# Kernel tuning notes

Measured on AMD Instinct MI355X. Metric: run time of the kernel, lower is better.

Reference implementation:

```python
import jax, jax.numpy as jnp
import numpy as np

H = 768
L = 9
M = 5            # max_span_length
CTX_RATIO = 0.5
NEG_INF = -1e30


def setup_inputs() -> dict:
    key = jax.random.key(0)
    ks = jax.random.split(key, 12)
    B, S = 4, 2048
    sc = 1.0 / np.sqrt(H)
    return {
        "sequence_output": jax.random.normal(ks[0], (B, S, H), dtype=jnp.float32),
        "Wc": jax.random.normal(ks[1], (H, L), dtype=jnp.float32) * sc,
        "bc": jnp.zeros((L,), dtype=jnp.float32),
        "wa": jax.random.normal(ks[2], (H,), dtype=jnp.float32) * sc,
        "ba": jnp.zeros((), dtype=jnp.float32),
        "W1": jax.random.normal(ks[3], (2 * H, H), dtype=jnp.float32) * (1.0 / np.sqrt(2 * H)),
        "b1": jnp.zeros((H,), dtype=jnp.float32),
        "gamma": jnp.ones((H,), dtype=jnp.float32),
        "beta": jnp.zeros((H,), dtype=jnp.float32),
        "W2": jax.random.normal(ks[4], (H, L), dtype=jnp.float32) * sc,
        "b2": jnp.zeros((L,), dtype=jnp.float32),
    }


def reference(sequence_output, Wc, bc, wa, ba, W1, b1, gamma, beta, W2, b2):
    x = sequence_output                        # [B,S,H]
    B, S, _ = x.shape
    base_logits = jnp.einsum('bsh,hl->bsl', x, Wc) + bc   # [B,S,L]

    # sliding-window indices: window [i-M, i+M] clipped to [0, S)
    offsets = jnp.arange(-M, M + 1)            # [W]
    idx = jnp.arange(S)[:, None] + offsets     # [S,W]
    valid = (idx >= 0) & (idx < S)             # [S,W]
    idx_c = jnp.clip(idx, 0, S - 1)            # [S,W]

    # attention scores over window (span_attention linear -> scalar per token)
    scores = jnp.einsum('bsh,h->bs', x, wa) + ba           # [B,S]
    win_scores = scores[:, idx_c]                          # [B,S,W]
    win_scores = jnp.where(valid[None], win_scores, NEG_INF)
    attn = jax.nn.softmax(win_scores, axis=-1)             # [B,S,W]

    win_tokens = x[:, idx_c]                               # [B,S,W,H] gather
    weighted_ctx = jnp.einsum('bsw,bswh->bsh', attn, win_tokens)

    token_with_ctx = jnp.concatenate([x, weighted_ctx], axis=-1)  # [B,S,2H]
    h = jnp.einsum('bsd,dh->bsh', token_with_ctx, W1) + b1
    # LayerNorm (eps = 1e-5, torch default)
    mu = jnp.mean(h, axis=-1, keepdims=True)
    var = jnp.mean((h - mu) ** 2, axis=-1, keepdims=True)
    h = (h - mu) * jax.lax.rsqrt(var + 1e-5) * gamma + beta
    h = jax.nn.gelu(h, approximate=False)                  # torch nn.GELU default (erf)
    ctx_logits = jnp.einsum('bsh,hl->bsl', h, W2) + b2

    return (1.0 - CTX_RATIO) * base_logits + CTX_RATIO * ctx_logits
```

## Files before the change

kernel.cpp:

```cpp
#include <hip/hip_runtime.h>
#include <hip/hip_bf16.h>
#include <math.h>

#define S_LEN 2048
#define BATCH 4
#define HDIM 768
#define LOUT 9
#define NROWS (BATCH*S_LEN)
#define K2H 1536
#define KHALF 768
#define WIN 11
#define NEG_INF_F (-1e30f)

typedef __attribute__((ext_vector_type(4))) float f32x4;
typedef __attribute__((ext_vector_type(8))) short bf16x8;

static __device__ __forceinline__ void async_ld16(const void* g, void* l) {
  __builtin_amdgcn_global_load_lds((const __attribute__((address_space(1))) void*)g,
                                   (__attribute__((address_space(3))) void*)l, 16, 0, 0);
}

static __device__ __forceinline__ unsigned short f2bf(float f) {
  union { float f; unsigned int u; } v; v.f = f;
  unsigned int u = v.u;
  unsigned int r = (u + 0x7fffu + ((u >> 16) & 1u)) >> 16;
  return (unsigned short)r;
}

static __device__ __forceinline__ float bf2f(unsigned short h) {
  union { unsigned int u; float f; } v; v.u = ((unsigned int)h) << 16;
  return v.f;
}

__global__ __launch_bounds__(256) void k_prep_w1t(const float* __restrict__ W1,
                                                  unsigned short* __restrict__ W1t) {
  __shared__ float tile[32][33];
  int bk = blockIdx.x % 48;
  int bn = blockIdx.x / 48;
  int tc = threadIdx.x % 32;
  int tr = threadIdx.x / 32;
  #pragma unroll
  for (int i = 0; i < 32; i += 8) {
    tile[tr + i][tc] = W1[(bk*32 + tr + i) * HDIM + bn*32 + tc];
  }
  __syncthreads();
  #pragma unroll
  for (int i = 0; i < 32; i += 8) {
    W1t[(bn*32 + tr + i) * K2H + bk*32 + tc] = f2bf(tile[tc][tr + i]);
  }
}

__global__ __launch_bounds__(192) void k_prep(const float* __restrict__ x,
                                              const float* __restrict__ wa,
                                              const float* __restrict__ ba,
                                              const float* __restrict__ Wc,
                                              const float* __restrict__ bc,
                                              unsigned short* __restrict__ xc,
                                              float* __restrict__ scores,
                                              float* __restrict__ base) {
  __shared__ float red[3][LOUT + 1];
  int bid = blockIdx.x;
  int row = (bid & 7) * 1024 + (bid >> 3);
  int t = threadIdx.x;
  int lane = t & 63, wave = t >> 6;
  const float4 v = *(const float4*)(x + row * HDIM + t * 4);
  const float4 w = *(const float4*)(wa + t * 4);
  ushort4 o;
  o.x = f2bf(v.x); o.y = f2bf(v.y); o.z = f2bf(v.z); o.w = f2bf(v.w);
  *(ushort4*)(xc + row * K2H + t * 4) = o;

  float pv[LOUT + 1];
  pv[LOUT] = v.x * w.x + v.y * w.y + v.z * w.z + v.w * w.w;
  #pragma unroll
  for (int l = 0; l < LOUT; ++l) pv[l] = 0.f;
  const float xvv[4] = { v.x, v.y, v.z, v.w };
  #pragma unroll
  for (int j = 0; j < 4; ++j) {
    const float* wr = Wc + (t * 4 + j) * LOUT;
    #pragma unroll
    for (int l = 0; l < LOUT; ++l) pv[l] += xvv[j] * wr[l];
  }
  #pragma unroll
  for (int l = 0; l <= LOUT; ++l)
    #pragma unroll
    for (int m = 1; m < 64; m <<= 1) pv[l] += __shfl_xor(pv[l], m);
  if (lane == 0) {
    #pragma unroll
    for (int l = 0; l <= LOUT; ++l) red[wave][l] = pv[l];
  }
  __syncthreads();
  if (t < LOUT) {
    base[row * LOUT + t] = red[0][t] + red[1][t] + red[2][t] + bc[t];
  } else if (t == LOUT) {
    scores[row] = red[0][LOUT] + red[1][LOUT] + red[2][LOUT] + ba[0];
  }
}

__global__ __launch_bounds__(192) void k_ctx(const float* __restrict__ scores,
                                             unsigned short* __restrict__ xc) {
  __shared__ float swin[WIN];
  int bid = blockIdx.x;
  int row = (bid & 7) * 1024 + (bid >> 3);
  int b = row >> 11, s = row & 2047;
  int t = threadIdx.x;
  if (t < WIN) {
    int j = s - 5 + t;
    bool valid = (j >= 0) && (j < S_LEN);
    int jc = valid ? j : (j < 0 ? 0 : S_LEN - 1);
    swin[t] = valid ? scores[b * S_LEN + jc] : NEG_INF_F;
  }
  __syncthreads();
  float mx = swin[0];
  #pragma unroll
  for (int w = 1; w < WIN; ++w) mx = fmaxf(mx, swin[w]);
  float es[WIN], ssum = 0.f;
  #pragma unroll
  for (int w = 0; w < WIN; ++w) {
    float sv = swin[w];
    es[w] = (sv > -1e29f) ? __expf(sv - mx) : 0.f;
    ssum += es[w];
  }
  float inv = 1.f / ssum;
  float c0 = 0.f, c1 = 0.f, c2 = 0.f, c3 = 0.f;
  #pragma unroll
  for (int w = 0; w < WIN; ++w) {
    float aw = es[w] * inv;
    int j = s - 5 + w;
    int jc = (j < 0) ? 0 : ((j >= S_LEN) ? S_LEN - 1 : j);
    const ushort4 uv = *(const ushort4*)(xc + (((long)b * S_LEN + jc) * K2H) + t * 4);
    c0 += aw * bf2f(uv.x);
    c1 += aw * bf2f(uv.y);
    c2 += aw * bf2f(uv.z);
    c3 += aw * bf2f(uv.w);
  }
  ushort4 o;
  o.x = f2bf(c0); o.y = f2bf(c1); o.z = f2bf(c2); o.w = f2bf(c3);
  *(ushort4*)(xc + row * K2H + HDIM + t * 4) = o;
}

__global__ __launch_bounds__(256, 3) void k_gemm(const unsigned short* __restrict__ A,
                                                 const unsigned short* __restrict__ Bt,
                                                 unsigned short* __restrict__ Hout) {
  __shared__ unsigned short As[2][128 * 32];
  __shared__ unsigned short Bs[2][128 * 32];
  int bid = blockIdx.x;
  int obid = (bid & 7) * 96 + (bid >> 3);
  int kh = obid / 384;
  int mt = obid % 384;
  int bm = mt / 6, bn = mt % 6;
  int t = threadIdx.x;
  int lane = t & 63, wave = t >> 6;
  int wm = wave >> 1, wn = wave & 1;

  int rowc = lane >> 2;
  int fST = ((lane >> 2) ^ (lane >> 4)) & 3;
  int sST = (lane & 3) ^ fST;
  const unsigned short* gA0 = A  + (long)(bm * 128 + wave * 16 + rowc) * K2H + kh * KHALF + sST * 8;
  const unsigned short* gB0 = Bt + (long)(bn * 128 + wave * 16 + rowc) * K2H + kh * KHALF + sST * 8;

  int fR = ((lane & 3) ^ ((lane >> 2) & 3)) & 3;
  int slR = ((lane >> 4) ^ fR) & 3;
  int arow = wm * 64 + (lane & 15);
  int brow = wn * 64 + (lane & 15);

  f32x4 acc[4][4] = {};

#define STAGE(buf, kt) do {                                                    \
    async_ld16(gA0 + (kt),            &As[buf][(wave * 16) * 32]);             \
    async_ld16(gA0 + 64 * K2H + (kt), &As[buf][(64 + wave * 16) * 32]);        \
    async_ld16(gB0 + (kt),            &Bs[buf][(wave * 16) * 32]);             \
    async_ld16(gB0 + 64 * K2H + (kt), &Bs[buf][(64 + wave * 16) * 32]);        \
  } while (0)

#define COMPUTE(buf) do {                                                      \
    bf16x8 af[4], bfv[4];                                                      \
    _Pragma("unroll")                                                          \
    for (int m = 0; m < 4; ++m)                                                \
      af[m] = *(const bf16x8*)(&As[buf][(arow + m * 16) * 32 + slR * 8]);      \
    _Pragma("unroll")                                                          \
    for (int n = 0; n < 4; ++n)                                                \
      bfv[n] = *(const bf16x8*)(&Bs[buf][(brow + n * 16) * 32 + slR * 8]);     \
    _Pragma("unroll")                                                          \
    for (int m = 0; m < 4; ++m)                                                \
      _Pragma("unroll")                                                        \
      for (int n = 0; n < 4; ++n)                                              \
        acc[m][n] = __builtin_amdgcn_mfma_f32_16x16x32_bf16(af[m], bfv[n], acc[m][n], 0, 0, 0); \
  } while (0)

  STAGE(0, 0);
  __syncthreads();
  int cur = 0;
  #pragma unroll 1
  for (int tt = 0; tt < 23; ++tt) {
    STAGE(cur ^ 1, (tt + 1) * 32);
    COMPUTE(cur);
    __syncthreads();
    cur ^= 1;
  }
  COMPUTE(cur);

  unsigned short* Hp = Hout + (long)kh * NROWS * HDIM;
  int orow = bm * 128 + wm * 64 + (lane >> 4) * 4;
  int ocol = bn * 128 + wn * 64 + (lane & 15);
  #pragma unroll
  for (int m = 0; m < 4; ++m)
    #pragma unroll
    for (int n = 0; n < 4; ++n) {
      int col = ocol + n * 16;
      #pragma unroll
      for (int r = 0; r < 4; ++r) {
        Hp[(long)(orow + m * 16 + r) * HDIM + col] = f2bf(acc[m][n][r]);
      }
    }
#undef STAGE
#undef COMPUTE
}

__global__ __launch_bounds__(192) void k_ln(const unsigned short* __restrict__ H0,
                                            const unsigned short* __restrict__ H1,
                                            const float* __restrict__ b1,
                                            const float* __restrict__ gamma,
                                            const float* __restrict__ beta,
                                            const float* __restrict__ W2,
                                            const float* __restrict__ b2,
                                            const float* __restrict__ base,
                                            float* __restrict__ out) {
  __shared__ float redS[3], redQ[3], redp[3][LOUT];
  int row = blockIdx.x;
  int t = threadIdx.x;
  int lane = t & 63, wave = t >> 6;
  const ushort4 h0 = *(const ushort4*)(H0 + (long)row * HDIM + t * 4);
  const ushort4 h1 = *(const ushort4*)(H1 + (long)row * HDIM + t * 4);
  const float4 b14 = *(const float4*)(b1 + t * 4);
  const float vv[4] = { bf2f(h0.x) + bf2f(h1.x) + b14.x,
                        bf2f(h0.y) + bf2f(h1.y) + b14.y,
                        bf2f(h0.z) + bf2f(h1.z) + b14.z,
                        bf2f(h0.w) + bf2f(h1.w) + b14.w };
  float s1 = vv[0] + vv[1] + vv[2] + vv[3];
  float s2 = vv[0]*vv[0] + vv[1]*vv[1] + vv[2]*vv[2] + vv[3]*vv[3];
  #pragma unroll
  for (int m = 1; m < 64; m <<= 1) { s1 += __shfl_xor(s1, m); s2 += __shfl_xor(s2, m); }
  if (lane == 0) { redS[wave] = s1; redQ[wave] = s2; }
  __syncthreads();
  s1 = redS[0] + redS[1] + redS[2];
  s2 = redQ[0] + redQ[1] + redQ[2];
  float mu = s1 * (1.f / HDIM);
  float var = s2 * (1.f / HDIM) - mu * mu;
  float rstd = rsqrtf(var + 1e-5f);
  const float4 g4 = *(const float4*)(gamma + t * 4);
  const float4 be4 = *(const float4*)(beta + t * 4);
  const float gv[4] = { g4.x, g4.y, g4.z, g4.w };
  const float bvv[4] = { be4.x, be4.y, be4.z, be4.w };
  float p[LOUT] = {};
  #pragma unroll
  for (int j = 0; j < 4; ++j) {
    float g = (vv[j] - mu) * rstd * gv[j] + bvv[j];
    float gg = 0.5f * g * (1.f + erff(g * 0.70710678118654752f));
    const float* wrow = W2 + (t * 4 + j) * LOUT;
    #pragma unroll
    for (int l = 0; l < LOUT; ++l) p[l] += gg * wrow[l];
  }
  #pragma unroll
  for (int l = 0; l < LOUT; ++l)
    #pragma unroll
    for (int m = 1; m < 64; m <<= 1) p[l] += __shfl_xor(p[l], m);
  if (lane == 0) {
    #pragma unroll
    for (int l = 0; l < LOUT; ++l) redp[wave][l] = p[l];
  }
  __syncthreads();
  if (t < LOUT) {
    float cl = redp[0][t] + redp[1][t] + redp[2][t] + b2[t];
    out[row * LOUT + t] = 0.5f * base[row * LOUT + t] + 0.5f * cl;
  }
}

extern "C" void kernel_launch(void* const* d_in, const int* in_sizes, int n_in,
                              void* d_out, int out_size, void* d_ws, size_t ws_size,
                              hipStream_t stream) {
  const float* x     = (const float*)d_in[0];
  const float* Wc    = (const float*)d_in[1];
  const float* bc    = (const float*)d_in[2];
  const float* wa    = (const float*)d_in[3];
  const float* ba    = (const float*)d_in[4];
  const float* W1    = (const float*)d_in[5];
  const float* b1    = (const float*)d_in[6];
  const float* gamma = (const float*)d_in[7];
  const float* beta  = (const float*)d_in[8];
  const float* W2    = (const float*)d_in[9];
  const float* b2    = (const float*)d_in[10];
  float* out = (float*)d_out;

  char* ws = (char*)d_ws;
  unsigned short* xc   = (unsigned short*)(ws);
  unsigned short* w1t  = (unsigned short*)(ws + 25165824);
  float* scores        = (float*)(ws + 27525120);
  float* base          = (float*)(ws + 27557888);
  unsigned short* hbuf = (unsigned short*)(ws + 27852800);

  k_prep_w1t<<<dim3(1152), dim3(256), 0, stream>>>(W1, w1t);
  k_prep    <<<dim3(8192), dim3(192), 0, stream>>>(x, wa, ba, Wc, bc, xc, scores, base);
  k_ctx     <<<dim3(8192), dim3(192), 0, stream>>>(scores, xc);
  k_gemm    <<<dim3(768),  dim3(256), 0, stream>>>(xc, w1t, hbuf);
  k_ln      <<<dim3(8192), dim3(192), 0, stream>>>(hbuf, hbuf + (long)NROWS * HDIM, b1,
                                                   gamma, beta, W2, b2, base, out);
}
```

Before: 174.3 us.

## Map one wave per row in row kernels and merge W1 transpose into prep

```diff
diff --git a/kernel.cpp b/kernel.cpp
--- a/kernel.cpp
+++ b/kernel.cpp
@@ -32,25 +32,9 @@
   return v.f;
 }
 
-__global__ __launch_bounds__(256) void k_prep_w1t(const float* __restrict__ W1,
-                                                  unsigned short* __restrict__ W1t) {
-  __shared__ float tile[32][33];
-  int bk = blockIdx.x % 48;
-  int bn = blockIdx.x / 48;
-  int tc = threadIdx.x % 32;
-  int tr = threadIdx.x / 32;
-  #pragma unroll
-  for (int i = 0; i < 32; i += 8) {
-    tile[tr + i][tc] = W1[(bk*32 + tr + i) * HDIM + bn*32 + tc];
-  }
-  __syncthreads();
-  #pragma unroll
-  for (int i = 0; i < 32; i += 8) {
-    W1t[(bn*32 + tr + i) * K2H + bk*32 + tc] = f2bf(tile[tc][tr + i]);
-  }
-}
-
-__global__ __launch_bounds__(192) void k_prep(const float* __restrict__ x,
+__global__ __launch_bounds__(256) void k_prep(const float* __restrict__ W1,
+                                              unsigned short* __restrict__ W1t,
+                                              const float* __restrict__ x,
                                               const float* __restrict__ wa,
                                               const float* __restrict__ ba,
                                               const float* __restrict__ Wc,
@@ -58,84 +42,117 @@
                                               unsigned short* __restrict__ xc,
                                               float* __restrict__ scores,
                                               float* __restrict__ base) {
-  __shared__ float red[3][LOUT + 1];
-  int bid = blockIdx.x;
-  int row = (bid & 7) * 1024 + (bid >> 3);
-  int t = threadIdx.x;
-  int lane = t & 63, wave = t >> 6;
-  const float4 v = *(const float4*)(x + row * HDIM + t * 4);
-  const float4 w = *(const float4*)(wa + t * 4);
-  ushort4 o;
-  o.x = f2bf(v.x); o.y = f2bf(v.y); o.z = f2bf(v.z); o.w = f2bf(v.w);
-  *(ushort4*)(xc + row * K2H + t * 4) = o;
-
-  float pv[LOUT + 1];
-  pv[LOUT] = v.x * w.x + v.y * w.y + v.z * w.z + v.w * w.w;
-  #pragma unroll
-  for (int l = 0; l < LOUT; ++l) pv[l] = 0.f;
-  const float xvv[4] = { v.x, v.y, v.z, v.w };
-  #pragma unroll
-  for (int j = 0; j < 4; ++j) {
-    const float* wr = Wc + (t * 4 + j) * LOUT;
-    #pragma unroll
-    for (int l = 0; l < LOUT; ++l) pv[l] += xvv[j] * wr[l];
-  }
-  #pragma unroll
-  for (int l = 0; l <= LOUT; ++l)
-    #pragma unroll
-    for (int m = 1; m < 64; m <<= 1) pv[l] += __shfl_xor(pv[l], m);
+  __shared__ float tile[32][33];
+  if (blockIdx.x < 1152) {
+    int bk = blockIdx.x % 48;
+    int bn = blockIdx.x / 48;
+    int tc = threadIdx.x % 32;
+    int tr = threadIdx.x / 32;
+    #pragma unroll
+    for (int i = 0; i < 32; i += 8) {
+      tile[tr + i][tc] = W1[(bk*32 + tr + i) * HDIM + bn*32 + tc];
+    }
+    __syncthreads();
+    #pragma unroll
+    for (int i = 0; i < 32; i += 8) {
+      W1t[(bn*32 + tr + i) * K2H + bk*32 + tc] = f2bf(tile[tc][tr + i]);
+    }
+    return;
+  }
+  int bid = blockIdx.x - 1152;
+  int lane = threadIdx.x & 63, wave = threadIdx.x >> 6;
+  int row = bid * 4 + wave;
+  const float* xr = x + (long)row * HDIM + lane * 12;
+  float xv[12];
+  { const float4 a = *(const float4*)(xr);
+    const float4 b4 = *(const float4*)(xr + 4);
+    const float4 c4 = *(const float4*)(xr + 8);
+    xv[0]=a.x; xv[1]=a.y; xv[2]=a.z; xv[3]=a.w;
+    xv[4]=b4.x; xv[5]=b4.y; xv[6]=b4.z; xv[7]=b4.w;
+    xv[8]=c4.x; xv[9]=c4.y; xv[10]=c4.z; xv[11]=c4.w; }
+  unsigned short* dst = xc + (long)row * K2H + lane * 12;
+  #pragma unroll
+  for (int q = 0; q < 3; ++q) {
+    ushort4 o;
+    o.x = f2bf(xv[q*4+0]); o.y = f2bf(xv[q*4+1]);
+    o.z = f2bf(xv[q*4+2]); o.w = f2bf(xv[q*4+3]);
+    *(ushort4*)(dst + q*4) = o;
+  }
+  const float* war = wa + lane * 12;
+  float sc = 0.f;
+  #pragma unroll
+  for (int q = 0; q < 3; ++q) {
+    const float4 w4 = *(const float4*)(war + q*4);
+    sc += xv[q*4+0]*w4.x + xv[q*4+1]*w4.y + xv[q*4+2]*w4.z + xv[q*4+3]*w4.w;
+  }
+  const float* wcr = Wc + (long)lane * 12 * LOUT;
+  float p[LOUT] = {};
+  #pragma unroll
+  for (int j = 0; j < 12; ++j) {
+    const float xj = xv[j];
+    #pragma unroll
+    for (int l = 0; l < LOUT; ++l) p[l] += xj * wcr[j * LOUT + l];
+  }
+  #pragma unroll
+  for (int m = 1; m < 64; m <<= 1) {
+    sc += __shfl_xor(sc, m);
+    #pragma unroll
+    for (int l = 0; l < LOUT; ++l) p[l] += __shfl_xor(p[l], m);
+  }
   if (lane == 0) {
-    #pragma unroll
-    for (int l = 0; l <= LOUT; ++l) red[wave][l] = pv[l];
-  }
-  __syncthreads();
-  if (t < LOUT) {
-    base[row * LOUT + t] = red[0][t] + red[1][t] + red[2][t] + bc[t];
-  } else if (t == LOUT) {
-    scores[row] = red[0][LOUT] + red[1][LOUT] + red[2][LOUT] + ba[0];
-  }
-}
-
-__global__ __launch_bounds__(192) void k_ctx(const float* __restrict__ scores,
+    scores[row] = sc + ba[0];
+    #pragma unroll
+    for (int l = 0; l < LOUT; ++l) base[row * LOUT + l] = p[l] + bc[l];
+  }
+}
+
+__global__ __launch_bounds__(256) void k_ctx(const float* __restrict__ scores,
                                              unsigned short* __restrict__ xc) {
-  __shared__ float swin[WIN];
-  int bid = blockIdx.x;
-  int row = (bid & 7) * 1024 + (bid >> 3);
+  int lane = threadIdx.x & 63, wave = threadIdx.x >> 6;
+  int row = blockIdx.x * 4 + wave;
   int b = row >> 11, s = row & 2047;
-  int t = threadIdx.x;
-  if (t < WIN) {
-    int j = s - 5 + t;
+  float sw[WIN];
+  int jcs[WIN];
+  #pragma unroll
+  for (int w = 0; w < WIN; ++w) {
+    int j = s - 5 + w;
     bool valid = (j >= 0) && (j < S_LEN);
     int jc = valid ? j : (j < 0 ? 0 : S_LEN - 1);
-    swin[t] = valid ? scores[b * S_LEN + jc] : NEG_INF_F;
-  }
-  __syncthreads();
-  float mx = swin[0];
-  #pragma unroll
-  for (int w = 1; w < WIN; ++w) mx = fmaxf(mx, swin[w]);
+    jcs[w] = b * S_LEN + jc;
+    sw[w] = valid ? scores[b * S_LEN + jc] : NEG_INF_F;
+  }
+  float mx = sw[0];
+  #pragma unroll
+  for (int w = 1; w < WIN; ++w) mx = fmaxf(mx, sw[w]);
   float es[WIN], ssum = 0.f;
   #pragma unroll
   for (int w = 0; w < WIN; ++w) {
-    float sv = swin[w];
-    es[w] = (sv > -1e29f) ? __expf(sv - mx) : 0.f;
+    es[w] = (sw[w] > -1e29f) ? __expf(sw[w] - mx) : 0.f;
     ssum += es[w];
   }
   float inv = 1.f / ssum;
-  float c0 = 0.f, c1 = 0.f, c2 = 0.f, c3 = 0.f;
+  float c[12] = {};
   #pragma unroll
   for (int w = 0; w < WIN; ++w) {
     float aw = es[w] * inv;
-    int j = s - 5 + w;
-    int jc = (j < 0) ? 0 : ((j >= S_LEN) ? S_LEN - 1 : j);
-    const ushort4 uv = *(const ushort4*)(xc + (((long)b * S_LEN + jc) * K2H) + t * 4);
-    c0 += aw * bf2f(uv.x);
-    c1 += aw * bf2f(uv.y);
-    c2 += aw * bf2f(uv.z);
-    c3 += aw * bf2f(uv.w);
-  }
-  ushort4 o;
-  o.x = f2bf(c0); o.y = f2bf(c1); o.z = f2bf(c2); o.w = f2bf(c3);
-  *(ushort4*)(xc + row * K2H + HDIM + t * 4) = o;
+    const unsigned short* src = xc + (long)jcs[w] * K2H + lane * 12;
+    #pragma unroll
+    for (int q = 0; q < 3; ++q) {
+      const ushort4 uv = *(const ushort4*)(src + q*4);
+      c[q*4+0] += aw * bf2f(uv.x);
+      c[q*4+1] += aw * bf2f(uv.y);
+      c[q*4+2] += aw * bf2f(uv.z);
+      c[q*4+3] += aw * bf2f(uv.w);
+    }
+  }
+  unsigned short* dst = xc + (long)row * K2H + HDIM + lane * 12;
+  #pragma unroll
+  for (int q = 0; q < 3; ++q) {
+    ushort4 o;
+    o.x = f2bf(c[q*4+0]); o.y = f2bf(c[q*4+1]);
+    o.z = f2bf(c[q*4+2]); o.w = f2bf(c[q*4+3]);
+    *(ushort4*)(dst + q*4) = o;
+  }
 }
 
 __global__ __launch_bounds__(256, 3) void k_gemm(const unsigned short* __restrict__ A,
@@ -216,7 +233,7 @@
 #undef COMPUTE
 }
 
-__global__ __launch_bounds__(192) void k_ln(const unsigned short* __restrict__ H0,
+__global__ __launch_bounds__(256) void k_ln(const unsigned short* __restrict__ H0,
                                             const unsigned short* __restrict__ H1,
                                             const float* __restrict__ b1,
                                             const float* __restrict__ gamma,
@@ -225,53 +242,58 @@
                                             const float* __restrict__ b2,
                                             const float* __restrict__ base,
                                             float* __restrict__ out) {
-  __shared__ float redS[3], redQ[3], redp[3][LOUT];
-  int row = blockIdx.x;
-  int t = threadIdx.x;
-  int lane = t & 63, wave = t >> 6;
-  const ushort4 h0 = *(const ushort4*)(H0 + (long)row * HDIM + t * 4);
-  const ushort4 h1 = *(const ushort4*)(H1 + (long)row * HDIM + t * 4);
-  const float4 b14 = *(const float4*)(b1 + t * 4);
-  const float vv[4] = { bf2f(h0.x) + bf2f(h1.x) + b14.x,
-                        bf2f(h0.y) + bf2f(h1.y) + b14.y,
-                        bf2f(h0.z) + bf2f(h1.z) + b14.z,
-                        bf2f(h0.w) + bf2f(h1.w) + b14.w };
-  float s1 = vv[0] + vv[1] + vv[2] + vv[3];
-  float s2 = vv[0]*vv[0] + vv[1]*vv[1] + vv[2]*vv[2] + vv[3]*vv[3];
+  int lane = threadIdx.x & 63, wave = threadIdx.x >> 6;
+  int row = blockIdx.x * 4 + wave;
+  const unsigned short* h0p = H0 + (long)row * HDIM + lane * 12;
+  const unsigned short* h1p = H1 + (long)row * HDIM + lane * 12;
+  const float* b1p = b1 + lane * 12;
+  float vv[12];
+  #pragma unroll
+  for (int q = 0; q < 3; ++q) {
+    const ushort4 a = *(const ushort4*)(h0p + q*4);
+    const ushort4 b4 = *(const ushort4*)(h1p + q*4);
+    const float4 bb = *(const float4*)(b1p + q*4);
+    vv[q*4+0] = bf2f(a.x) + bf2f(b4.x) + bb.x;
+    vv[q*4+1] = bf2f(a.y) + bf2f(b4.y) + bb.y;
+    vv[q*4+2] = bf2f(a.z) + bf2f(b4.z) + bb.z;
+    vv[q*4+3] = bf2f(a.w) + bf2f(b4.w) + bb.w;
+  }
+  float s1 = 0.f, s2 = 0.f;
+  #pragma unroll
+  for (int j = 0; j < 12; ++j) { s1 += vv[j]; s2 += vv[j] * vv[j]; }
   #pragma unroll
   for (int m = 1; m < 64; m <<= 1) { s1 += __shfl_xor(s1, m); s2 += __shfl_xor(s2, m); }
-  if (lane == 0) { redS[wave] = s1; redQ[wave] = s2; }
-  __syncthreads();
-  s1 = redS[0] + redS[1] + redS[2];
-  s2 = redQ[0] + redQ[1] + redQ[2];
   float mu = s1 * (1.f / HDIM);
   float var = s2 * (1.f / HDIM) - mu * mu;
   float rstd = rsqrtf(var + 1e-5f);
-  const float4 g4 = *(const float4*)(gamma + t * 4);
-  const float4 be4 = *(const float4*)(beta + t * 4);
-  const float gv[4] = { g4.x, g4.y, g4.z, g4.w };
-  const float bvv[4] = { be4.x, be4.y, be4.z, be4.w };
+  const float* gp = gamma + lane * 12;
+  const float* bp = beta + lane * 12;
+  const float* w2r = W2 + (long)lane * 12 * LOUT;
   float p[LOUT] = {};
   #pragma unroll
-  for (int j = 0; j < 4; ++j) {
-    float g = (vv[j] - mu) * rstd * gv[j] + bvv[j];
-    float gg = 0.5f * g * (1.f + erff(g * 0.70710678118654752f));
-    const float* wrow = W2 + (t * 4 + j) * LOUT;
-    #pragma unroll
-    for (int l = 0; l < LOUT; ++l) p[l] += gg * wrow[l];
-  }
-  #pragma unroll
-  for (int l = 0; l < LOUT; ++l)
-    #pragma unroll
-    for (int m = 1; m < 64; m <<= 1) p[l] += __shfl_xor(p[l], m);
+  for (int q = 0; q < 3; ++q) {
+    const float4 g4 = *(const float4*)(gp + q*4);
+    const float4 be4 = *(const float4*)(bp + q*4);
+    const float gv[4] = { g4.x, g4.y, g4.z, g4.w };
+    const float bvv[4] = { be4.x, be4.y, be4.z, be4.w };
+    #pragma unroll
+    for (int k = 0; k < 4; ++k) {
+      int j = q*4 + k;
+      float g = (vv[j] - mu) * rstd * gv[k] + bvv[k];
+      float gg = 0.5f * g * (1.f + erff(g * 0.70710678118654752f));
+      #pragma unroll
+      for (int l = 0; l < LOUT; ++l) p[l] += gg * w2r[j * LOUT + l];
+    }
+  }
+  #pragma unroll
+  for (int m = 1; m < 64; m <<= 1)
+    #pragma unroll
+    for (int l = 0; l < LOUT; ++l) p[l] += __shfl_xor(p[l], m);
   if (lane == 0) {
     #pragma unroll
-    for (int l = 0; l < LOUT; ++l) redp[wave][l] = p[l];
-  }
-  __syncthreads();
-  if (t < LOUT) {
-    float cl = redp[0][t] + redp[1][t] + redp[2][t] + b2[t];
-    out[row * LOUT + t] = 0.5f * base[row * LOUT + t] + 0.5f * cl;
+    for (int l = 0; l < LOUT; ++l) {
+      out[row * LOUT + l] = 0.5f * base[row * LOUT + l] + 0.5f * (p[l] + b2[l]);
+    }
   }
 }
 
@@ -298,10 +320,10 @@
   float* base          = (float*)(ws + 27557888);
   unsigned short* hbuf = (unsigned short*)(ws + 27852800);
 
-  k_prep_w1t<<<dim3(1152), dim3(256), 0, stream>>>(W1, w1t);
-  k_prep    <<<dim3(8192), dim3(192), 0, stream>>>(x, wa, ba, Wc, bc, xc, scores, base);
-  k_ctx     <<<dim3(8192), dim3(192), 0, stream>>>(scores, xc);
-  k_gemm    <<<dim3(768),  dim3(256), 0, stream>>>(xc, w1t, hbuf);
-  k_ln      <<<dim3(8192), dim3(192), 0, stream>>>(hbuf, hbuf + (long)NROWS * HDIM, b1,
-                                                   gamma, beta, W2, b2, base, out);
-}
+  k_prep <<<dim3(1152 + 2048), dim3(256), 0, stream>>>(W1, w1t, x, wa, ba, Wc, bc,
+                                                       xc, scores, base);
+  k_ctx  <<<dim3(2048), dim3(256), 0, stream>>>(scores, xc);
+  k_gemm <<<dim3(768),  dim3(256), 0, stream>>>(xc, w1t, hbuf);
+  k_ln   <<<dim3(2048), dim3(256), 0, stream>>>(hbuf, hbuf + (long)NROWS * HDIM, b1,
+                                                gamma, beta, W2, b2, base, out);
+}
```

Measured after the change: 171.0 us (median of 2 runs). No clear change (-1.9%).
